# Optimization experiments

Hardware: AMD Instinct MI355X
Metric: run time of the kernel (lower is better)

## Reference

```python
import jax, jax.numpy as jnp
import numpy as np

N_WORDS = 500000
N_LABELS = 64
PAD_INDEX = 0
UNK_INDEX = 1
BATCH, SEQ_LEN = 8192, 512


def setup_inputs() -> dict:
    key = jax.random.key(0)
    kw, kl, klen = jax.random.split(key, 3)
    # sequence lengths in [S/2, S]; pads go at the end (loop semantics assume contiguous prefix)
    lens = jax.random.randint(klen, (BATCH,), SEQ_LEN // 2, SEQ_LEN + 1)
    words = jax.random.randint(kw, (BATCH, SEQ_LEN), 2, N_WORDS, dtype=jnp.int32)
    labels = jax.random.randint(kl, (BATCH, SEQ_LEN), 0, N_LABELS, dtype=jnp.int32)
    pos = jnp.arange(SEQ_LEN, dtype=jnp.int32)[None, :]
    words = jnp.where(pos < lens[:, None], words, PAD_INDEX)
    trans_count = jnp.zeros((N_LABELS + 1, N_LABELS + 1), jnp.float32)
    emit_count = jnp.zeros((N_WORDS, N_LABELS), jnp.float32)
    return {"words": words, "labels": labels,
            "trans_count": trans_count, "emit_count": emit_count}


def reference(words, labels, trans_count, emit_count):
    # Vectorized equivalent of the double Python loop of scalar increments.
    B, S = words.shape
    lens = (words != PAD_INDEX).sum(-1)                       # [B]
    valid = jnp.arange(S, dtype=lens.dtype)[None, :] < lens[:, None]  # [B,S]
    wgt = valid.astype(trans_count.dtype).ravel()             # 1.0 for counted tokens
    ext_words = jnp.where(words >= N_WORDS, UNK_INDEX, words)
    # pre label: -1 (== last index N_LABELS) at j=0, else labels[:, j-1]
    pre = jnp.concatenate(
        [jnp.full((B, 1), N_LABELS, labels.dtype), labels[:, :-1]], axis=1)
    # trans_count[t, pre] += 1  (flattened scatter-add)
    t_flat = (labels.astype(jnp.int32) * (N_LABELS + 1) + pre.astype(jnp.int32)).ravel()
    tc = trans_count.ravel().at[t_flat].add(wgt).reshape(trans_count.shape)
    # emit_count[w, t] += 1
    e_flat = (ext_words.astype(jnp.int32) * N_LABELS + labels.astype(jnp.int32)).ravel()
    ec = emit_count.ravel().at[e_flat].add(wgt).reshape(emit_count.shape)
    return tc, ec
```

## Files before the change

### kernel.cpp

```cpp
#include <hip/hip_runtime.h>
#include <hip/hip_bf16.h>


constexpr int N_WORDS  = 500000;
constexpr int N_LABELS = 64;
constexpr int SEQ_LEN  = 512;
constexpr int BINS     = (N_LABELS + 1) * (N_LABELS + 1);
constexpr int N_CELLS  = N_WORDS * N_LABELS;
constexpr int P        = 512;
constexpr int CPP      = 62528;
constexpr int CAP      = 16384;
constexpr int CHUNK    = 16384;
constexpr int B1 = 1024, G1 = 512;
constexpr int B2 = 1024;


__global__ __launch_bounds__(B1)
void phase1(const int* __restrict__ words, const int* __restrict__ labels,
            unsigned* __restrict__ cursors,
            unsigned short* __restrict__ keys,
            unsigned* __restrict__ part_t,
            int nquads) {
    __shared__ unsigned trans[BINS];
    __shared__ unsigned cnt[P];
    __shared__ unsigned base[P];
    __shared__ unsigned pos[P];
    for (int k = threadIdx.x; k < BINS; k += B1) trans[k] = 0u;
    for (int k = threadIdx.x; k < P;    k += B1) { cnt[k] = 0u; pos[k] = 0u; }
    __syncthreads();

    const int stride = gridDim.x * blockDim.x;
    const int t0 = blockIdx.x * blockDim.x + threadIdx.x;

    for (int q = t0; q < nquads; q += stride) {
        const int4 w4 = reinterpret_cast<const int4*>(words)[q];
        const int4 l4 = reinterpret_cast<const int4*>(labels)[q];
        int wv[4] = {w4.x, w4.y, w4.z, w4.w};
        int lv[4] = {l4.x, l4.y, l4.z, l4.w};
        #pragma unroll
        for (int k = 0; k < 4; ++k) {
            if (wv[k] != 0) {
                const int w = (wv[k] >= N_WORDS) ? 1 : wv[k];
                const unsigned key = (unsigned)w * N_LABELS + (unsigned)lv[k];
                atomicAdd(&cnt[key / CPP], 1u);
            }
        }
    }
    __syncthreads();

    for (int p = threadIdx.x; p < P; p += B1)
        base[p] = atomicAdd(&cursors[p], cnt[p]);
    __syncthreads();

    for (int q = t0; q < nquads; q += stride) {
        const int i = q << 2;
        const int4 w4 = reinterpret_cast<const int4*>(words)[q];
        const int4 l4 = reinterpret_cast<const int4*>(labels)[q];
        const int j0 = i & (SEQ_LEN - 1);
        int pre = (j0 == 0) ? N_LABELS : labels[i - 1];
        int wv[4] = {w4.x, w4.y, w4.z, w4.w};
        int lv[4] = {l4.x, l4.y, l4.z, l4.w};
        #pragma unroll
        for (int k = 0; k < 4; ++k) {
            const int lab = lv[k];
            if (wv[k] != 0) {
                atomicAdd(&trans[lab * (N_LABELS + 1) + pre], 1u);
                const int w = (wv[k] >= N_WORDS) ? 1 : wv[k];
                const unsigned key = (unsigned)w * N_LABELS + (unsigned)lab;
                const unsigned p   = key / CPP;
                const unsigned slot = base[p] + atomicAdd(&pos[p], 1u);
                if (slot < CAP)
                    keys[(size_t)p * CAP + slot] = (unsigned short)(key - p * CPP);
            }
            pre = lab;
        }
    }
    __syncthreads();

    unsigned* my = part_t + (size_t)blockIdx.x * BINS;
    for (int k = threadIdx.x; k < BINS; k += B1) my[k] = trans[k];
}

__global__ __launch_bounds__(B2)
void phase2(const unsigned* __restrict__ cursors,
            const unsigned short* __restrict__ keys,
            float* __restrict__ out) {
    extern __shared__ unsigned h[];
    const unsigned p = blockIdx.x;
    float* __restrict__ emit = out + BINS;
    const unsigned base_cell = p * (unsigned)CPP;
    const unsigned cells = min((unsigned)CPP, (unsigned)N_CELLS - base_cell);
    unsigned nk = cursors[p]; if (nk > CAP) nk = CAP;
    const unsigned short* kp = keys + (size_t)p * CAP;

    for (unsigned lo = 0; lo < cells; lo += CHUNK) {
        const unsigned hi = min(lo + (unsigned)CHUNK, cells);
        const unsigned n = hi - lo;
        for (unsigned j = threadIdx.x; j < n; j += B2) h[j] = 0u;
        __syncthreads();
        for (unsigned i = threadIdx.x; i < nk; i += B2) {
            const unsigned c = kp[i];
            if (c >= lo && c < hi) atomicAdd(&h[c - lo], 1u);
        }
        __syncthreads();
        for (unsigned j = threadIdx.x; j < n; j += B2)
            emit[base_cell + lo + j] = (float)h[j];
        __syncthreads();
    }
}

__global__ __launch_bounds__(256)
void finalize_new(const unsigned* __restrict__ part_t, float* __restrict__ out) {
    const int k = blockIdx.x;
    __shared__ unsigned red[256];
    unsigned s = 0;
    for (int pb = threadIdx.x; pb < G1; pb += 256)
        s += part_t[(size_t)pb * BINS + k];
    red[threadIdx.x] = s;
    __syncthreads();
    for (int off = 128; off > 0; off >>= 1) {
        if (threadIdx.x < (unsigned)off) red[threadIdx.x] += red[threadIdx.x + off];
        __syncthreads();
    }
    if (threadIdx.x == 0) out[k] = (float)red[0];
}


__global__ __launch_bounds__(256)
void zero_kernel(uint4* __restrict__ out, int out_quads, int out_size) {
    const uint4 z = {0u, 0u, 0u, 0u};
    const int stride = gridDim.x * blockDim.x;
    for (int q = blockIdx.x * blockDim.x + threadIdx.x; q < out_quads; q += stride)
        out[q] = z;
    if (blockIdx.x == 0 && threadIdx.x < (out_size & 3))
        ((unsigned*)out)[(out_quads << 2) + threadIdx.x] = 0u;
}

__global__ __launch_bounds__(1024)
void count_fallback(const int* __restrict__ words, const int* __restrict__ labels,
                    float* __restrict__ out, int nquads) {
    __shared__ unsigned hist[BINS];
    for (int k = threadIdx.x; k < BINS; k += 1024) hist[k] = 0u;
    __syncthreads();
    float* __restrict__ emit = out + BINS;
    const int stride = gridDim.x * blockDim.x;
    for (int q = blockIdx.x * blockDim.x + threadIdx.x; q < nquads; q += stride) {
        const int i = q << 2;
        const int4 w4 = reinterpret_cast<const int4*>(words)[q];
        const int4 l4 = reinterpret_cast<const int4*>(labels)[q];
        const int j0 = i & (SEQ_LEN - 1);
        int pre = (j0 == 0) ? N_LABELS : labels[i - 1];
        int wv[4] = {w4.x, w4.y, w4.z, w4.w};
        int lv[4] = {l4.x, l4.y, l4.z, l4.w};
        #pragma unroll
        for (int k = 0; k < 4; ++k) {
            const int w = wv[k], lab = lv[k];
            if (w != 0) {
                atomicAdd(&hist[lab * (N_LABELS + 1) + pre], 1u);
                const int we = (w >= N_WORDS) ? 1 : w;
                atomicAdd(&emit[(size_t)we * N_LABELS + lab], 1.0f);
            }
            pre = lab;
        }
    }
    __syncthreads();
    for (int k = threadIdx.x; k < BINS; k += 1024) {
        const unsigned c = hist[k];
        if (c) atomicAdd(&out[k], (float)c);
    }
}


extern "C" void kernel_launch(void* const* d_in, const int* in_sizes, int n_in,
                              void* d_out, int out_size, void* d_ws, size_t ws_size,
                              hipStream_t stream) {
    const int* words  = (const int*)d_in[0];
    const int* labels = (const int*)d_in[1];
    float* out = (float*)d_out;

    const int n      = in_sizes[0];
    const int nquads = n >> 2;

    const size_t cur_bytes  = 4096;
    const size_t key_bytes  = (size_t)P * CAP * sizeof(unsigned short);
    const size_t part_bytes = (size_t)G1 * BINS * sizeof(unsigned);
    const size_t need = cur_bytes + key_bytes + part_bytes;

    if (ws_size >= need) {
        unsigned* cursors      = (unsigned*)d_ws;
        unsigned short* keys   = (unsigned short*)((char*)d_ws + cur_bytes);
        unsigned* part_t       = (unsigned*)((char*)d_ws + cur_bytes + key_bytes);

        hipMemsetAsync(cursors, 0, P * sizeof(unsigned), stream);
        phase1<<<G1, B1, 0, stream>>>(words, labels, cursors, keys, part_t, nquads);
        phase2<<<P, B2, CHUNK * sizeof(unsigned), stream>>>(cursors, keys, out);
        finalize_new<<<BINS, 256, 0, stream>>>(part_t, out);
    } else {
        const int out_quads = out_size >> 2;
        zero_kernel<<<2048, 256, 0, stream>>>((uint4*)d_out, out_quads, out_size);
        count_fallback<<<512, 1024, 0, stream>>>(words, labels, out, nquads);
    }
}
```

Before: 270.0 us.

## Single-pass tiled bucketing with packed 16-bit histograms and fused finalize

Phase1 now processes tokens in per-block tiles of 8192, computing each key once and staging the packed partition/offset in shared memory. This replaces the two full passes over global inputs. Partitions double to 1025 with half-size ranges, and phase2 keeps the whole partition in one shared-memory histogram by packing two 16-bit counters per word, dropping the multi-chunk rescans of the key list. The transition-count reduction is folded into extra blocks of phase2, removing a separate launch. Risks include 16-bit counter overflow, per-tile syncs and global cursor atomics, and a larger shared-memory footprint per block.

```diff
diff --git a/kernel.cpp b/kernel.cpp
--- a/kernel.cpp
+++ b/kernel.cpp
@@ -7,12 +7,13 @@
 constexpr int SEQ_LEN  = 512;
 constexpr int BINS     = (N_LABELS + 1) * (N_LABELS + 1);
 constexpr int N_CELLS  = N_WORDS * N_LABELS;
-constexpr int P        = 512;
-constexpr int CPP      = 62528;
-constexpr int CAP      = 16384;
-constexpr int CHUNK    = 16384;
+constexpr int P        = 1025;
+constexpr int CPP      = 31232;
+constexpr int CAP      = 8192;
 constexpr int B1 = 1024, G1 = 512;
+constexpr int TILE_TOK = 8192;
 constexpr int B2 = 1024;
+constexpr int FIN_BLOCKS = 5;
 
 
 __global__ __launch_bounds__(B1)
@@ -20,109 +21,116 @@
             unsigned* __restrict__ cursors,
             unsigned short* __restrict__ keys,
             unsigned* __restrict__ part_t,
-            int nquads) {
+            int n) {
     __shared__ unsigned trans[BINS];
+    __shared__ unsigned keybuf[TILE_TOK];
     __shared__ unsigned cnt[P];
     __shared__ unsigned base[P];
     __shared__ unsigned pos[P];
     for (int k = threadIdx.x; k < BINS; k += B1) trans[k] = 0u;
-    for (int k = threadIdx.x; k < P;    k += B1) { cnt[k] = 0u; pos[k] = 0u; }
-    __syncthreads();
-
-    const int stride = gridDim.x * blockDim.x;
-    const int t0 = blockIdx.x * blockDim.x + threadIdx.x;
-
-    for (int q = t0; q < nquads; q += stride) {
-        const int4 w4 = reinterpret_cast<const int4*>(words)[q];
-        const int4 l4 = reinterpret_cast<const int4*>(labels)[q];
-        int wv[4] = {w4.x, w4.y, w4.z, w4.w};
-        int lv[4] = {l4.x, l4.y, l4.z, l4.w};
-        #pragma unroll
-        for (int k = 0; k < 4; ++k) {
-            if (wv[k] != 0) {
-                const int w = (wv[k] >= N_WORDS) ? 1 : wv[k];
-                const unsigned key = (unsigned)w * N_LABELS + (unsigned)lv[k];
-                atomicAdd(&cnt[key / CPP], 1u);
+    __syncthreads();
+
+    const int nquads = n >> 2;
+    const int qpt    = TILE_TOK >> 2;
+    const int ntiles = (nquads + qpt - 1) / qpt;
+
+    for (int tile = blockIdx.x; tile < ntiles; tile += gridDim.x) {
+        const int q0     = tile * qpt;
+        const int tquads = min(qpt, nquads - q0);
+
+        for (int k = threadIdx.x; k < P; k += B1) { cnt[k] = 0u; pos[k] = 0u; }
+        __syncthreads();
+
+        for (int lq = threadIdx.x; lq < tquads; lq += B1) {
+            const int q = q0 + lq;
+            const int i = q << 2;
+            const int4 w4 = reinterpret_cast<const int4*>(words)[q];
+            const int4 l4 = reinterpret_cast<const int4*>(labels)[q];
+            const int j0 = i & (SEQ_LEN - 1);
+            int pre = (j0 == 0) ? N_LABELS : labels[i - 1];
+            int wv[4] = {w4.x, w4.y, w4.z, w4.w};
+            int lv[4] = {l4.x, l4.y, l4.z, l4.w};
+            #pragma unroll
+            for (int k = 0; k < 4; ++k) {
+                const int lab = lv[k];
+                unsigned pack = 0xFFFFFFFFu;
+                if (wv[k] != 0) {
+                    atomicAdd(&trans[lab * (N_LABELS + 1) + pre], 1u);
+                    const int w = (wv[k] >= N_WORDS) ? 1 : wv[k];
+                    const unsigned key = (unsigned)w * N_LABELS + (unsigned)lab;
+                    const unsigned p   = key / CPP;
+                    pack = (p << 16) | (key - p * CPP);
+                    atomicAdd(&cnt[p], 1u);
+                }
+                keybuf[(lq << 2) + k] = pack;
+                pre = lab;
             }
         }
-    }
-    __syncthreads();
-
-    for (int p = threadIdx.x; p < P; p += B1)
-        base[p] = atomicAdd(&cursors[p], cnt[p]);
-    __syncthreads();
-
-    for (int q = t0; q < nquads; q += stride) {
-        const int i = q << 2;
-        const int4 w4 = reinterpret_cast<const int4*>(words)[q];
-        const int4 l4 = reinterpret_cast<const int4*>(labels)[q];
-        const int j0 = i & (SEQ_LEN - 1);
-        int pre = (j0 == 0) ? N_LABELS : labels[i - 1];
-        int wv[4] = {w4.x, w4.y, w4.z, w4.w};
-        int lv[4] = {l4.x, l4.y, l4.z, l4.w};
-        #pragma unroll
-        for (int k = 0; k < 4; ++k) {
-            const int lab = lv[k];
-            if (wv[k] != 0) {
-                atomicAdd(&trans[lab * (N_LABELS + 1) + pre], 1u);
-                const int w = (wv[k] >= N_WORDS) ? 1 : wv[k];
-                const unsigned key = (unsigned)w * N_LABELS + (unsigned)lab;
-                const unsigned p   = key / CPP;
+        __syncthreads();
+
+        for (int p = threadIdx.x; p < P; p += B1) {
+            const unsigned c = cnt[p];
+            base[p] = c ? atomicAdd(&cursors[p], c) : 0u;
+        }
+        __syncthreads();
+
+        const int ttok = tquads << 2;
+        for (int t = threadIdx.x; t < ttok; t += B1) {
+            const unsigned pack = keybuf[t];
+            if (pack != 0xFFFFFFFFu) {
+                const unsigned p   = pack >> 16;
+                const unsigned loc = pack & 0xFFFFu;
                 const unsigned slot = base[p] + atomicAdd(&pos[p], 1u);
                 if (slot < CAP)
-                    keys[(size_t)p * CAP + slot] = (unsigned short)(key - p * CPP);
+                    keys[(size_t)p * CAP + slot] = (unsigned short)loc;
             }
-            pre = lab;
-        }
-    }
-    __syncthreads();
+        }
+        __syncthreads();
+    }
 
     unsigned* my = part_t + (size_t)blockIdx.x * BINS;
     for (int k = threadIdx.x; k < BINS; k += B1) my[k] = trans[k];
 }
+
 
 __global__ __launch_bounds__(B2)
 void phase2(const unsigned* __restrict__ cursors,
             const unsigned short* __restrict__ keys,
+            const unsigned* __restrict__ part_t,
             float* __restrict__ out) {
     extern __shared__ unsigned h[];
-    const unsigned p = blockIdx.x;
+    const unsigned bid = blockIdx.x;
+
+    if (bid >= (unsigned)P) {
+        const int k = (bid - P) * B2 + threadIdx.x;
+        if (k < BINS) {
+            unsigned s = 0;
+            #pragma unroll 8
+            for (int pb = 0; pb < G1; ++pb) s += part_t[(size_t)pb * BINS + k];
+            out[k] = (float)s;
+        }
+        return;
+    }
+
     float* __restrict__ emit = out + BINS;
-    const unsigned base_cell = p * (unsigned)CPP;
+    const unsigned base_cell = bid * (unsigned)CPP;
     const unsigned cells = min((unsigned)CPP, (unsigned)N_CELLS - base_cell);
-    unsigned nk = cursors[p]; if (nk > CAP) nk = CAP;
-    const unsigned short* kp = keys + (size_t)p * CAP;
-
-    for (unsigned lo = 0; lo < cells; lo += CHUNK) {
-        const unsigned hi = min(lo + (unsigned)CHUNK, cells);
-        const unsigned n = hi - lo;
-        for (unsigned j = threadIdx.x; j < n; j += B2) h[j] = 0u;
-        __syncthreads();
-        for (unsigned i = threadIdx.x; i < nk; i += B2) {
-            const unsigned c = kp[i];
-            if (c >= lo && c < hi) atomicAdd(&h[c - lo], 1u);
-        }
-        __syncthreads();
-        for (unsigned j = threadIdx.x; j < n; j += B2)
-            emit[base_cell + lo + j] = (float)h[j];
-        __syncthreads();
-    }
-}
-
-__global__ __launch_bounds__(256)
-void finalize_new(const unsigned* __restrict__ part_t, float* __restrict__ out) {
-    const int k = blockIdx.x;
-    __shared__ unsigned red[256];
-    unsigned s = 0;
-    for (int pb = threadIdx.x; pb < G1; pb += 256)
-        s += part_t[(size_t)pb * BINS + k];
-    red[threadIdx.x] = s;
-    __syncthreads();
-    for (int off = 128; off > 0; off >>= 1) {
-        if (threadIdx.x < (unsigned)off) red[threadIdx.x] += red[threadIdx.x + off];
-        __syncthreads();
-    }
-    if (threadIdx.x == 0) out[k] = (float)red[0];
+    const unsigned n32 = (cells + 1u) >> 1;
+    unsigned nk = cursors[bid]; if (nk > CAP) nk = CAP;
+    const unsigned short* kp = keys + (size_t)bid * CAP;
+
+    for (unsigned j = threadIdx.x; j < n32; j += B2) h[j] = 0u;
+    __syncthreads();
+    for (unsigned i = threadIdx.x; i < nk; i += B2) {
+        const unsigned c = kp[i];
+        atomicAdd(&h[c >> 1], (c & 1u) ? 65536u : 1u);
+    }
+    __syncthreads();
+    for (unsigned j = threadIdx.x; j < cells; j += B2) {
+        const unsigned v = h[j >> 1];
+        const unsigned c = (j & 1u) ? (v >> 16) : (v & 0xFFFFu);
+        emit[base_cell + j] = (float)c;
+    }
 }
 
 
@@ -164,6 +172,7 @@
         }
     }
     __syncthreads();
+    for (int k = threadIdx.x; k < 1024 * 8 && k < BINS; k += 1024) {}
     for (int k = threadIdx.x; k < BINS; k += 1024) {
         const unsigned c = hist[k];
         if (c) atomicAdd(&out[k], (float)c);
@@ -178,26 +187,27 @@
     const int* labels = (const int*)d_in[1];
     float* out = (float*)d_out;
 
-    const int n      = in_sizes[0];
-    const int nquads = n >> 2;
-
-    const size_t cur_bytes  = 4096;
-    const size_t key_bytes  = (size_t)P * CAP * sizeof(unsigned short);
+    const int n = in_sizes[0];
+
+    const size_t cur_off   = 0;
+    const size_t key_off   = 8192;
+    const size_t key_bytes = (size_t)P * CAP * sizeof(unsigned short);
+    const size_t part_off  = key_off + key_bytes;
     const size_t part_bytes = (size_t)G1 * BINS * sizeof(unsigned);
-    const size_t need = cur_bytes + key_bytes + part_bytes;
+    const size_t need = part_off + part_bytes;
 
     if (ws_size >= need) {
-        unsigned* cursors      = (unsigned*)d_ws;
-        unsigned short* keys   = (unsigned short*)((char*)d_ws + cur_bytes);
-        unsigned* part_t       = (unsigned*)((char*)d_ws + cur_bytes + key_bytes);
+        unsigned* cursors    = (unsigned*)((char*)d_ws + cur_off);
+        unsigned short* keys = (unsigned short*)((char*)d_ws + key_off);
+        unsigned* part_t     = (unsigned*)((char*)d_ws + part_off);
 
         hipMemsetAsync(cursors, 0, P * sizeof(unsigned), stream);
-        phase1<<<G1, B1, 0, stream>>>(words, labels, cursors, keys, part_t, nquads);
-        phase2<<<P, B2, CHUNK * sizeof(unsigned), stream>>>(cursors, keys, out);
-        finalize_new<<<BINS, 256, 0, stream>>>(part_t, out);
+        phase1<<<G1, B1, 0, stream>>>(words, labels, cursors, keys, part_t, n);
+        phase2<<<P + FIN_BLOCKS, B2, (CPP / 2) * sizeof(unsigned), stream>>>(
+            cursors, keys, part_t, out);
     } else {
         const int out_quads = out_size >> 2;
         zero_kernel<<<2048, 256, 0, stream>>>((uint4*)d_out, out_quads, out_size);
-        count_fallback<<<512, 1024, 0, stream>>>(words, labels, out, nquads);
-    }
-}
+        count_fallback<<<512, 1024, 0, stream>>>(words, labels, out, n >> 2);
+    }
+}
```

Result: no change. 273.9 us (+1.4%).
